# Optimization experiments

Hardware: AMD Instinct MI355X
Metric: run time of the kernel (lower is better)

The kernel has to match this reference:

```python
import jax, jax.numpy as jnp
import numpy as np

B, A, C, M, E = 8, 100000, 8, 128, 32
ALPHA, GAMMA = 0.25, 2.0


def setup_inputs() -> dict:
    key = jax.random.key(0)
    k1, k2, k3, k4, k5, k6, k7 = jax.random.split(key, 7)
    classifications = jax.random.uniform(k1, (B, A, C), dtype=jnp.float32)
    regressions = jax.random.normal(k2, (B, A, 8), dtype=jnp.float32)
    embeddings = jax.random.normal(k3, (B, A, E), dtype=jnp.float32)
    # anchors: random centers on a 1920x1080 image, reasonable w/h -> x1,y1,x2,y2
    cx = jax.random.uniform(k4, (A,), minval=0.0, maxval=1920.0)
    cy = jax.random.uniform(jax.random.fold_in(k4, 1), (A,), minval=0.0, maxval=1080.0)
    w = jax.random.uniform(jax.random.fold_in(k4, 2), (A,), minval=16.0, maxval=256.0)
    h = jax.random.uniform(jax.random.fold_in(k4, 3), (A,), minval=16.0, maxval=256.0)
    anchors = jnp.stack([cx - 0.5 * w, cy - 0.5 * h, cx + 0.5 * w, cy + 0.5 * h], axis=1)[None].astype(jnp.float32)
    # annotations: 16 coords = jittered 3D-box corner projections around a random box,
    # col 16 = object id, col 17 = class label in [0, C)
    bcx = jax.random.uniform(k5, (B, M, 1), minval=100.0, maxval=1820.0)
    bcy = jax.random.uniform(jax.random.fold_in(k5, 1), (B, M, 1), minval=100.0, maxval=980.0)
    bw = jax.random.uniform(jax.random.fold_in(k5, 2), (B, M, 1), minval=30.0, maxval=300.0)
    bh = jax.random.uniform(jax.random.fold_in(k5, 3), (B, M, 1), minval=30.0, maxval=300.0)
    jit = jax.random.uniform(k6, (B, M, 16), minval=-0.4, maxval=0.4)
    sx = jnp.array([-1, -1, 1, 1, -1, -1, 1, 1], jnp.float32)
    sy = jnp.array([-1, 1, -1, 1, -1, 1, -1, 1], jnp.float32)
    xs = bcx + 0.5 * bw * (sx + jit[..., 0:16:2])
    ys = bcy + 0.5 * bh * (sy + jit[..., 1:16:2])
    coords = jnp.stack([xs, ys], axis=-1).reshape(B, M, 16)
    ids = jax.random.randint(k7, (B, M, 1), 0, 1000).astype(jnp.float32)
    cls_lab = jax.random.randint(jax.random.fold_in(k7, 1), (B, M, 1), 0, C).astype(jnp.float32)
    annotations = jnp.concatenate([coords, ids, cls_lab], axis=-1)
    return {
        "classifications": classifications,
        "regressions": regressions,
        "anchors": anchors,
        "annotations": annotations,
        "embeddings": embeddings,
    }


def calc_iou(a, b):
    # a: [A,4], b: [M,4] in x1,y1,x2,y2 -> [A,M]
    area = (b[:, 2] - b[:, 0]) * (b[:, 3] - b[:, 1])
    iw = jnp.minimum(a[:, 2:3], b[None, :, 2]) - jnp.maximum(a[:, 0:1], b[None, :, 0])
    ih = jnp.minimum(a[:, 3:4], b[None, :, 3]) - jnp.maximum(a[:, 1:2], b[None, :, 1])
    iw = jnp.clip(iw, 0.0)
    ih = jnp.clip(ih, 0.0)
    ua = ((a[:, 2] - a[:, 0]) * (a[:, 3] - a[:, 1]))[:, None] + area[None, :] - iw * ih
    return iw * ih / jnp.clip(ua, 1e-8)


_S2 = jnp.array([-1, -1, 1, 1, -1, -1, 1, 1], jnp.float32)
_S4 = jnp.array([-1, 1, -1, 1, -1, 1, -1, 1], jnp.float32)
_S6 = jnp.array([1, 1, 1, 1, -1, -1, -1, -1], jnp.float32)


def _per_image(cls, reg, ann, anchor):
    # cls [A,C], reg [A,8], ann [M,18], anchor [A,4]
    aw = anchor[:, 2] - anchor[:, 0]
    ah = anchor[:, 3] - anchor[:, 1]
    acx = anchor[:, 0] + 0.5 * aw
    acy = anchor[:, 1] + 0.5 * ah
    cls = jnp.clip(cls, 1e-4, 1.0 - 1e-4)
    valid = ann[:, -1] >= 0.0  # [M]; annotations with class -1 are padding
    xs, ys = ann[:, 0:16:2], ann[:, 1:16:2]
    box2d = jnp.stack([xs.min(1), ys.min(1), xs.max(1), ys.max(1)], axis=1)  # [M,4]
    iou = jnp.where(valid[None, :], calc_iou(anchor, box2d), -1.0)  # [A,M]
    iou_max = iou.max(1)
    assigned = ann[iou.argmax(1)]  # [A,18]
    pos = iou_max >= 0.5
    neg = iou_max < 0.4
    num_pos = jnp.maximum(pos.sum().astype(cls.dtype), 1.0)

    onehot = jax.nn.one_hot(assigned[:, -1].astype(jnp.int32), cls.shape[1], dtype=cls.dtype)
    targets = jnp.where(pos[:, None], onehot, jnp.where(neg[:, None], 0.0, -1.0))
    alpha_f = jnp.where(targets == 1.0, ALPHA, 1.0 - ALPHA)
    focal_w = alpha_f * jnp.where(targets == 1.0, 1.0 - cls, cls) ** GAMMA
    bce = -(targets * jnp.log(cls) + (1.0 - targets) * jnp.log(1.0 - cls))
    cls_loss = jnp.where(targets != -1.0, focal_w * bce, 0.0).sum() / num_pos

    t = assigned[:, :16]

    def vp(rx, ry, tx, ty):
        denom = jnp.sqrt(rx * rx + ry * ry) * jnp.sqrt(tx * tx + ty * ty)
        return 1.0 - (rx * tx + ry * ty) / jnp.maximum(denom, 1e-8)

    vp1 = vp(reg[:, 2], reg[:, 3],
             (t[:, 4] + t[:, 6] + t[:, 12] + t[:, 14] - (t[:, 0] + t[:, 2] + t[:, 8] + t[:, 10])) / 4.0,
             (t[:, 5] + t[:, 7] + t[:, 13] + t[:, 15] - (t[:, 1] + t[:, 3] + t[:, 9] + t[:, 11])) / 4.0)
    vp2 = vp(reg[:, 4], reg[:, 5],
             (t[:, 2] + t[:, 6] + t[:, 10] + t[:, 14] - (t[:, 0] + t[:, 4] + t[:, 8] + t[:, 12])) / 4.0,
             (t[:, 3] + t[:, 7] + t[:, 11] + t[:, 15] - (t[:, 1] + t[:, 5] + t[:, 9] + t[:, 13])) / 4.0)
    vp3 = vp(reg[:, 6], reg[:, 7],
             (t[:, 0] + t[:, 2] + t[:, 4] + t[:, 6] - (t[:, 8] + t[:, 10] + t[:, 12] + t[:, 14])) / 4.0,
             (t[:, 1] + t[:, 3] + t[:, 5] + t[:, 7] - (t[:, 9] + t[:, 11] + t[:, 13] + t[:, 15])) / 4.0)
    vp_all = (vp1 + vp2 + vp3) / 3.0
    vp_loss = (vp_all * pos).sum() / num_pos

    # corner predictions from (ctr_x, ctr_y, v1, v2, v3) offsets: [A,8] x-coords, [A,8] y-coords
    px = reg[:, 0:1] + reg[:, 2:3] * _S2 + reg[:, 4:5] * _S4 + reg[:, 6:7] * _S6
    py = reg[:, 1:2] + reg[:, 3:4] * _S2 + reg[:, 5:6] * _S4 + reg[:, 7:8] * _S6
    tx = (t[:, 0:16:2] - acx[:, None]) / aw[:, None]
    ty = (t[:, 1:16:2] - acy[:, None]) / ah[:, None]
    diff = jnp.concatenate([jnp.abs(px - tx), jnp.abs(py - ty)], axis=1)  # [A,16]
    sl1 = jnp.where(diff <= 1.0 / 9.0, 0.5 * 9.0 * diff * diff, diff - 0.5 / 9.0)
    reg_loss = (sl1.mean(1) * pos).sum() / num_pos
    return cls_loss, reg_loss, vp_loss


def reference(classifications, regressions, anchors, annotations, embeddings):
    anchor = anchors[0]
    cls_l, reg_l, vp_l = jax.vmap(_per_image, in_axes=(0, 0, 0, None))(
        classifications, regressions, annotations, anchor)
    return jnp.stack([cls_l.mean(), reg_l.mean(), vp_l.mean()])


if __name__ == "__main__":
    print(reference(**setup_inputs()))
```

## Files before the change

kernel.cpp:

```cpp
#include <hip/hip_runtime.h>

namespace {

constexpr int B_N = 8;
constexpr int A_N = 100000;
constexpr int M_N = 128;
constexpr int BLOCK = 256;
constexpr int NBLK_S = (A_N + BLOCK - 1) / BLOCK;
constexpr int GX = 16, GY = 9, NC = GX * GY;
constexpr float CELL = 120.0f;
constexpr float MARGIN = 128.0f;
constexpr int CPC = 4;
constexpr int NCH = NC * CPC;

constexpr size_t OFF_BOX  = 0;
constexpr size_t OFF_MASK = OFF_BOX + (size_t)B_N * M_N * 8 * 4;
constexpr size_t OFF_HIST = OFF_MASK + (size_t)B_N * NC * 2 * 8;
constexpr size_t OFF_OFFS = OFF_HIST + (size_t)NBLK_S * NC * 4;
constexpr size_t OFF_CT   = OFF_OFFS + (size_t)NC * NBLK_S * 4;
constexpr size_t OFF_CB   = OFF_CT + NC * 4;
constexpr size_t OFF_SIDX = (OFF_CB + (NC + 1) * 4 + 15) & ~size_t(15);
constexpr size_t OFF_SANC = (OFF_SIDX + (size_t)A_N * 4 + 15) & ~size_t(15);
constexpr size_t OFF_PART = OFF_SANC + (size_t)A_N * 16;

__device__ __forceinline__ int cell_of(const float4& an) {
    const float acx = 0.5f * (an.x + an.z);
    const float acy = 0.5f * (an.y + an.w);
    const int cx = min(GX - 1, max(0, (int)(acx * (1.0f / CELL))));
    const int cy = min(GY - 1, max(0, (int)(acy * (1.0f / CELL))));
    return cy * GX + cx;
}

__global__ void k0_prep(const float* __restrict__ ann_, float* __restrict__ boxbuf)
{
    const int i = blockIdx.x * blockDim.x + threadIdx.x;
    if (i >= B_N * M_N) return;
    const float* t = ann_ + (size_t)i * 18;
    float minx = t[0], maxx = t[0], miny = t[1], maxy = t[1];
#pragma unroll
    for (int j = 1; j < 8; ++j) {
        const float xj = t[2 * j], yj = t[2 * j + 1];
        minx = fminf(minx, xj); maxx = fmaxf(maxx, xj);
        miny = fminf(miny, yj); maxy = fmaxf(maxy, yj);
    }
    float area = (maxx - minx) * (maxy - miny);
    if (t[17] < 0.0f) {
        minx = 1e30f; miny = 1e30f; maxx = -1e30f; maxy = -1e30f; area = 0.0f;
    }
    float* o = boxbuf + (size_t)i * 8;
    o[0] = minx; o[1] = miny; o[2] = maxx; o[3] = maxy;
    o[4] = area; o[5] = 0.f;  o[6] = 0.f;  o[7] = 0.f;
}

__global__ void kmask(const float* __restrict__ boxbuf,
                      unsigned long long* __restrict__ maskbuf)
{
    const int cell = blockIdx.x, b = blockIdx.y, m = threadIdx.x;
    const int cx = cell % GX, cy = cell / GX;
    const float lox = cx * CELL - MARGIN, hix = cx * CELL + CELL + MARGIN;
    const float loy = cy * CELL - MARGIN, hiy = cy * CELL + CELL + MARGIN;
    const float* r = boxbuf + ((size_t)b * M_N + m) * 8;
    const bool ok = (r[0] <= hix) && (r[2] >= lox) && (r[1] <= hiy) && (r[3] >= loy);
    const unsigned long long bal = __ballot(ok);
    if ((m & 63) == 0)
        maskbuf[((size_t)b * NC + cell) * 2 + (m >> 6)] = bal;
}

__global__ __launch_bounds__(BLOCK) void s1_hist(
    const float* __restrict__ anchors_, unsigned* __restrict__ hist)
{
    __shared__ unsigned h[NC];
    const int tid = threadIdx.x, blk = blockIdx.x;
    for (int i = tid; i < NC; i += BLOCK) h[i] = 0u;
    __syncthreads();
    const int a = blk * BLOCK + tid;
    if (a < A_N) {
        const float4 an = ((const float4*)anchors_)[a];
        atomicAdd(&h[cell_of(an)], 1u);
    }
    __syncthreads();
    for (int i = tid; i < NC; i += BLOCK) hist[(size_t)blk * NC + i] = h[i];
}

__global__ __launch_bounds__(BLOCK) void s2a_scan(
    const unsigned* __restrict__ hist,
    unsigned* __restrict__ offs,
    unsigned* __restrict__ cellTot)
{
    const int c = blockIdx.x, t = threadIdx.x;
    const int k0 = 2 * t, k1 = 2 * t + 1;
    const unsigned v0 = (k0 < NBLK_S) ? hist[(size_t)k0 * NC + c] : 0u;
    const unsigned v1 = (k1 < NBLK_S) ? hist[(size_t)k1 * NC + c] : 0u;
    const unsigned mysum = v0 + v1;
    __shared__ unsigned s[BLOCK];
    s[t] = mysum;
    __syncthreads();
    for (int off = 1; off < BLOCK; off <<= 1) {
        const unsigned x = (t >= off) ? s[t - off] : 0u;
        __syncthreads();
        s[t] += x;
        __syncthreads();
    }
    const unsigned excl = s[t] - mysum;
    if (k0 < NBLK_S) offs[(size_t)c * NBLK_S + k0] = excl;
    if (k1 < NBLK_S) offs[(size_t)c * NBLK_S + k1] = excl + v0;
    if (t == BLOCK - 1) cellTot[c] = s[BLOCK - 1];
}

__global__ __launch_bounds__(BLOCK) void s2b_base(
    const unsigned* __restrict__ cellTot, unsigned* __restrict__ cellBase)
{
    __shared__ unsigned s[BLOCK];
    const int t = threadIdx.x;
    const unsigned v = (t < NC) ? cellTot[t] : 0u;
    s[t] = v;
    __syncthreads();
    for (int off = 1; off < BLOCK; off <<= 1) {
        const unsigned x = (t >= off) ? s[t - off] : 0u;
        __syncthreads();
        s[t] += x;
        __syncthreads();
    }
    if (t < NC) cellBase[t] = s[t] - v;
    if (t == NC - 1) cellBase[NC] = s[t];
}

__global__ __launch_bounds__(BLOCK) void s3_scatter(
    const float* __restrict__ anchors_,
    const unsigned* __restrict__ offs, const unsigned* __restrict__ cellBase,
    unsigned* __restrict__ sidx, float4* __restrict__ sanc)
{
    __shared__ int cellArr[BLOCK];
    const int tid = threadIdx.x, blk = blockIdx.x;
    const int a = blk * BLOCK + tid;
    const bool v = (a < A_N);
    float4 an = make_float4(0.f, 0.f, 0.f, 0.f);
    int c = -1;
    if (v) { an = ((const float4*)anchors_)[a]; c = cell_of(an); }
    cellArr[tid] = c;
    __syncthreads();
    if (v) {
        int rank = 0;
        for (int j = 0; j < tid; ++j) rank += (cellArr[j] == c);
        const unsigned d = cellBase[c] + offs[(size_t)c * NBLK_S + blk] + (unsigned)rank;
        sidx[d] = (unsigned)a;
        sanc[d] = an;
    }
}

__global__ __launch_bounds__(BLOCK) void ka2(
    const float* __restrict__ cls_,
    const float* __restrict__ reg_,
    const float* __restrict__ ann_,
    const float* __restrict__ boxbuf,
    const unsigned* __restrict__ maskbuf,
    const unsigned* __restrict__ cellBase,
    const unsigned* __restrict__ sidx,
    const float4* __restrict__ sanc,
    float* __restrict__ partials)
{
    const int cc = blockIdx.x / CPC, chunk = blockIdx.x % CPC;
    const int b = blockIdx.y, tid = threadIdx.x;
    const int base = (int)cellBase[cc];
    const int n    = (int)cellBase[cc + 1] - base;

    if (chunk * BLOCK >= n) {
        if (tid == 0) {
            float* o = partials + ((size_t)b * NCH + blockIdx.x) * 4;
            o[0] = 0.f; o[1] = 0.f; o[2] = 0.f; o[3] = 0.f;
        }
        return;
    }

    __shared__ float s_x1[M_N], s_y1[M_N], s_x2[M_N], s_y2[M_N], s_nb[M_N];
    __shared__ int   s_id[M_N];
    __shared__ unsigned s_mask[4], s_pre[4];
    __shared__ int s_Kv;
    __shared__ float s_ann[M_N * 18];

    for (int i = tid; i < M_N * 18; i += BLOCK)
        s_ann[i] = ann_[(size_t)b * M_N * 18 + i];
    if (tid < 4) s_mask[tid] = maskbuf[((size_t)b * NC + cc) * 4 + tid];
    __syncthreads();
    if (tid == 0) {
        unsigned p = 0;
#pragma unroll
        for (int w = 0; w < 4; ++w) { s_pre[w] = p; p += __popc(s_mask[w]); }
        s_Kv = (int)p;
    }
    __syncthreads();
    if (tid < M_N) {
        const unsigned w = s_mask[tid >> 5];
        if ((w >> (tid & 31)) & 1u) {
            const int r = (int)(s_pre[tid >> 5] + __popc(w & ((1u << (tid & 31)) - 1u)));
            const float* rec = boxbuf + ((size_t)b * M_N + tid) * 8;
            s_x1[r] = rec[0]; s_y1[r] = rec[1];
            s_x2[r] = rec[2]; s_y2[r] = rec[3];
            s_nb[r] = -rec[4];
            s_id[r] = tid;
        }
    }
    __syncthreads();
    const int K = s_Kv;

    const int i0  = chunk * BLOCK + tid;
    const bool inb = (i0 < n);
    const int gi  = base + (inb ? i0 : 0);
    const float4 an = sanc[gi];
    const int a = (int)sidx[gi];

    const float* cp = cls_ + ((size_t)b * A_N + a) * 8;
    const float4 cA = ((const float4*)cp)[0];
    const float4 cB = ((const float4*)cp)[1];

    const float aarea = (an.z - an.x) * (an.w - an.y);
    float m1 = -3e38f, m2 = -3e38f;
    float bn = 0.f, bs = 1.f;
    int   kb = 0;

    for (int m = 0; m < K; ++m) {
        const float x1 = s_x1[m], y1 = s_y1[m];
        const float x2 = s_x2[m], y2 = s_y2[m];
        const float nb = s_nb[m];
        const float iw = fminf(an.z, x2) - fmaxf(an.x, x1);
        const float ih = fminf(an.w, y2) - fmaxf(an.y, y1);
        const float in_ = fmaxf(iw, 0.f) * fmaxf(ih, 0.f);
        m1 = fmaxf(m1, __builtin_fmaf(3.0f, in_, nb));
        m2 = fmaxf(m2, __builtin_fmaf(3.5f, in_, nb));
        const float s = aarea - nb;
        const bool  u = (in_ * bs > bn * s);
        bn = u ? in_ : bn;
        bs = u ? s   : bs;
        kb = u ? m   : kb;
    }

    const bool pos = inb && (m1 >= aarea);
    const bool nonign = pos || (m2 < aarea);

    float clsS = 0.f, regS = 0.f, vpS = 0.f, posC = 0.f;
    const float pv[8] = {cA.x, cA.y, cA.z, cA.w, cB.x, cB.y, cB.z, cB.w};
    {
        float s = 0.f;
#pragma unroll
        for (int c = 0; c < 8; ++c) {
            const float p = fminf(fmaxf(pv[c], 1e-4f), 1.0f - 1e-4f);
            s += 0.75f * p * p * (-__logf(1.0f - p));
        }
        clsS = (inb && nonign) ? s : 0.f;
    }

    if (pos) {
        posC = 1.0f;
        const float* t = s_ann + s_id[kb] * 18;
        float tt[16];
#pragma unroll
        for (int j = 0; j < 16; ++j) tt[j] = t[j];
        const int kc = (int)t[17];

        float pkc = 0.5f;
#pragma unroll
        for (int c = 0; c < 8; ++c)
            if (c == kc) pkc = fminf(fmaxf(pv[c], 1e-4f), 1.0f - 1e-4f);
        const float negkc   = 0.75f * pkc * pkc * (-__logf(1.0f - pkc));
        const float posterm = 0.25f * (1.0f - pkc) * (1.0f - pkc) * (-__logf(pkc));
        clsS += posterm - negkc;

        const float aw = an.z - an.x;
        const float ah = an.w - an.y;
        const float* rp = reg_ + ((size_t)b * A_N + a) * 8;
        const float4 r0 = ((const float4*)rp)[0];
        const float4 r1 = ((const float4*)rp)[1];

        auto vp = [](float rx, float ry, float tx, float ty) {
            const float denom = sqrtf(rx * rx + ry * ry) * sqrtf(tx * tx + ty * ty);
            return 1.0f - (rx * tx + ry * ty) / fmaxf(denom, 1e-8f);
        };
        const float vp1 = vp(r0.z, r0.w,
            (tt[4] + tt[6] + tt[12] + tt[14] - (tt[0] + tt[2] + tt[8] + tt[10])) * 0.25f,
            (tt[5] + tt[7] + tt[13] + tt[15] - (tt[1] + tt[3] + tt[9] + tt[11])) * 0.25f);
        const float vp2 = vp(r1.x, r1.y,
            (tt[2] + tt[6] + tt[10] + tt[14] - (tt[0] + tt[4] + tt[8] + tt[12])) * 0.25f,
            (tt[3] + tt[7] + tt[11] + tt[15] - (tt[1] + tt[5] + tt[9] + tt[13])) * 0.25f);
        const float vp3 = vp(r1.z, r1.w,
            (tt[0] + tt[2] + tt[4] + tt[6] - (tt[8] + tt[10] + tt[12] + tt[14])) * 0.25f,
            (tt[1] + tt[3] + tt[5] + tt[7] - (tt[9] + tt[11] + tt[13] + tt[15])) * 0.25f);
        vpS = (vp1 + vp2 + vp3) * (1.0f / 3.0f);

        const float s2v[8] = {-1, -1, 1, 1, -1, -1, 1, 1};
        const float s4v[8] = {-1, 1, -1, 1, -1, 1, -1, 1};
        const float s6v[8] = {1, 1, 1, 1, -1, -1, -1, -1};
        const float acx2 = an.x + 0.5f * aw;
        const float acy2 = an.y + 0.5f * ah;
        float ssum = 0.f;
#pragma unroll
        for (int j = 0; j < 8; ++j) {
            const float px = r0.x + r0.z * s2v[j] + r1.x * s4v[j] + r1.z * s6v[j];
            const float py = r0.y + r0.w * s2v[j] + r1.y * s4v[j] + r1.w * s6v[j];
            const float tx = (tt[2 * j]     - acx2) / aw;
            const float ty = (tt[2 * j + 1] - acy2) / ah;
            const float dx = fabsf(px - tx);
            const float dy = fabsf(py - ty);
            ssum += (dx <= (1.0f / 9.0f)) ? 4.5f * dx * dx : dx - (0.5f / 9.0f);
            ssum += (dy <= (1.0f / 9.0f)) ? 4.5f * dy * dy : dy - (0.5f / 9.0f);
        }
        regS = ssum * (1.0f / 16.0f);
    }

#pragma unroll
    for (int off = 32; off; off >>= 1) {
        clsS += __shfl_down(clsS, off);
        regS += __shfl_down(regS, off);
        vpS  += __shfl_down(vpS, off);
        posC += __shfl_down(posC, off);
    }
    __shared__ float s_red[4][4];
    const int wv = tid >> 6, ln = tid & 63;
    if (ln == 0) {
        s_red[wv][0] = clsS; s_red[wv][1] = regS;
        s_red[wv][2] = vpS;  s_red[wv][3] = posC;
    }
    __syncthreads();
    if (tid == 0) {
        float C = 0, R = 0, V = 0, P = 0;
        for (int w2 = 0; w2 < 4; ++w2) {
            C += s_red[w2][0]; R += s_red[w2][1];
            V += s_red[w2][2]; P += s_red[w2][3];
        }
        float* out = partials + ((size_t)b * NCH + blockIdx.x) * 4;
        out[0] = C; out[1] = R; out[2] = V; out[3] = P;
    }
}

__global__ __launch_bounds__(BLOCK) void kc_final(
    const float* __restrict__ partials,
    float* __restrict__ out)
{
    const int tid = threadIdx.x;
    __shared__ float s[4][4];
    __shared__ float accum[3];
    if (tid == 0) { accum[0] = 0.f; accum[1] = 0.f; accum[2] = 0.f; }

    for (int b = 0; b < B_N; ++b) {
        float c = 0.f, r = 0.f, v = 0.f, p = 0.f;
        for (int i = tid; i < NCH; i += BLOCK) {
            const float* q = partials + ((size_t)b * NCH + i) * 4;
            c += q[0]; r += q[1]; v += q[2]; p += q[3];
        }
#pragma unroll
        for (int off = 32; off; off >>= 1) {
            c += __shfl_down(c, off); r += __shfl_down(r, off);
            v += __shfl_down(v, off); p += __shfl_down(p, off);
        }
        const int wv = tid >> 6, ln = tid & 63;
        if (ln == 0) { s[wv][0] = c; s[wv][1] = r; s[wv][2] = v; s[wv][3] = p; }
        __syncthreads();
        if (tid == 0) {
            float C = 0, R = 0, V = 0, P = 0;
            for (int w = 0; w < 4; ++w) {
                C += s[w][0]; R += s[w][1]; V += s[w][2]; P += s[w][3];
            }
            const float np_ = fmaxf(P, 1.0f);
            accum[0] += C / np_; accum[1] += R / np_; accum[2] += V / np_;
        }
        __syncthreads();
    }
    if (tid == 0) {
        out[0] = accum[0] * 0.125f;
        out[1] = accum[1] * 0.125f;
        out[2] = accum[2] * 0.125f;
    }
}

}

extern "C" void kernel_launch(void* const* d_in, const int* in_sizes, int n_in,
                              void* d_out, int out_size, void* d_ws, size_t ws_size,
                              hipStream_t stream)
{
    const float* cls_    = (const float*)d_in[0];
    const float* reg_    = (const float*)d_in[1];
    const float* anchors = (const float*)d_in[2];
    const float* ann     = (const float*)d_in[3];

    char* ws = (char*)d_ws;
    float*              boxbuf  = (float*)(ws + OFF_BOX);
    unsigned long long* maskbuf = (unsigned long long*)(ws + OFF_MASK);
    unsigned*           hist    = (unsigned*)(ws + OFF_HIST);
    unsigned*           offs    = (unsigned*)(ws + OFF_OFFS);
    unsigned*           cellTot = (unsigned*)(ws + OFF_CT);
    unsigned*           cellBase= (unsigned*)(ws + OFF_CB);
    unsigned*           sidxp   = (unsigned*)(ws + OFF_SIDX);
    float4*             sancp   = (float4*)(ws + OFF_SANC);
    float*              partials= (float*)(ws + OFF_PART);

    k0_prep<<<dim3((B_N * M_N + BLOCK - 1) / BLOCK), dim3(BLOCK), 0, stream>>>(ann, boxbuf);
    kmask<<<dim3(NC, B_N), dim3(M_N), 0, stream>>>(boxbuf, maskbuf);
    s1_hist<<<dim3(NBLK_S), dim3(BLOCK), 0, stream>>>(anchors, hist);
    s2a_scan<<<dim3(NC), dim3(BLOCK), 0, stream>>>(hist, offs, cellTot);
    s2b_base<<<dim3(1), dim3(BLOCK), 0, stream>>>(cellTot, cellBase);
    s3_scatter<<<dim3(NBLK_S), dim3(BLOCK), 0, stream>>>(anchors, offs, cellBase,
                                                         sidxp, sancp);
    ka2<<<dim3(NCH, B_N), dim3(BLOCK), 0, stream>>>(
        cls_, reg_, ann, boxbuf, (const unsigned*)maskbuf, cellBase,
        sidxp, sancp, partials);
    kc_final<<<dim3(1), dim3(BLOCK), 0, stream>>>(partials, (float*)d_out);
}
```

Measured before the change: 71.78 us.

## Fuse prep/mask and base-scan kernels, use wave-shuffle ranking in scatter

Merges the annotation box prep into the mask kernel and folds the single-block cell base scan into every scatter block, which drops two kernel launches. Each scatter block now recomputes the scan redundantly, and block 0 writes cellBase for ka2. The O(tid) shared-memory rank loop is replaced by a 64-iteration wave shuffle plus per-wave counts. ka2 no longer stages all annotations into shared memory and instead reads the matched annotation row from global memory, which adds scattered global loads for positive anchors.

```diff
diff --git a/kernel.cpp b/kernel.cpp
--- a/kernel.cpp
+++ b/kernel.cpp
@@ -31,11 +31,12 @@
     return cy * GX + cx;
 }
 
-__global__ void k0_prep(const float* __restrict__ ann_, float* __restrict__ boxbuf)
-{
-    const int i = blockIdx.x * blockDim.x + threadIdx.x;
-    if (i >= B_N * M_N) return;
-    const float* t = ann_ + (size_t)i * 18;
+__global__ void f0_prep_mask(const float* __restrict__ ann_,
+                             float* __restrict__ boxbuf,
+                             unsigned long long* __restrict__ maskbuf)
+{
+    const int cell = blockIdx.x, b = blockIdx.y, m = threadIdx.x;
+    const float* t = ann_ + ((size_t)b * M_N + m) * 18;
     float minx = t[0], maxx = t[0], miny = t[1], maxy = t[1];
 #pragma unroll
     for (int j = 1; j < 8; ++j) {
@@ -47,20 +48,15 @@
     if (t[17] < 0.0f) {
         minx = 1e30f; miny = 1e30f; maxx = -1e30f; maxy = -1e30f; area = 0.0f;
     }
-    float* o = boxbuf + (size_t)i * 8;
-    o[0] = minx; o[1] = miny; o[2] = maxx; o[3] = maxy;
-    o[4] = area; o[5] = 0.f;  o[6] = 0.f;  o[7] = 0.f;
-}
-
-__global__ void kmask(const float* __restrict__ boxbuf,
-                      unsigned long long* __restrict__ maskbuf)
-{
-    const int cell = blockIdx.x, b = blockIdx.y, m = threadIdx.x;
+    if (cell == 0) {
+        float* o = boxbuf + ((size_t)b * M_N + m) * 8;
+        o[0] = minx; o[1] = miny; o[2] = maxx; o[3] = maxy;
+        o[4] = area; o[5] = 0.f;  o[6] = 0.f;  o[7] = 0.f;
+    }
     const int cx = cell % GX, cy = cell / GX;
     const float lox = cx * CELL - MARGIN, hix = cx * CELL + CELL + MARGIN;
     const float loy = cy * CELL - MARGIN, hiy = cy * CELL + CELL + MARGIN;
-    const float* r = boxbuf + ((size_t)b * M_N + m) * 8;
-    const bool ok = (r[0] <= hix) && (r[2] >= lox) && (r[1] <= hiy) && (r[3] >= loy);
+    const bool ok = (minx <= hix) && (maxx >= lox) && (miny <= hiy) && (maxy >= loy);
     const unsigned long long bal = __ballot(ok);
     if ((m & 63) == 0)
         maskbuf[((size_t)b * NC + cell) * 2 + (m >> 6)] = bal;
@@ -107,42 +103,54 @@
     if (t == BLOCK - 1) cellTot[c] = s[BLOCK - 1];
 }
 
-__global__ __launch_bounds__(BLOCK) void s2b_base(
-    const unsigned* __restrict__ cellTot, unsigned* __restrict__ cellBase)
-{
-    __shared__ unsigned s[BLOCK];
-    const int t = threadIdx.x;
-    const unsigned v = (t < NC) ? cellTot[t] : 0u;
-    s[t] = v;
-    __syncthreads();
-    for (int off = 1; off < BLOCK; off <<= 1) {
-        const unsigned x = (t >= off) ? s[t - off] : 0u;
-        __syncthreads();
-        s[t] += x;
-        __syncthreads();
-    }
-    if (t < NC) cellBase[t] = s[t] - v;
-    if (t == NC - 1) cellBase[NC] = s[t];
-}
-
 __global__ __launch_bounds__(BLOCK) void s3_scatter(
     const float* __restrict__ anchors_,
-    const unsigned* __restrict__ offs, const unsigned* __restrict__ cellBase,
+    const unsigned* __restrict__ offs,
+    const unsigned* __restrict__ cellTot,
+    unsigned* __restrict__ cellBase,
     unsigned* __restrict__ sidx, float4* __restrict__ sanc)
 {
-    __shared__ int cellArr[BLOCK];
+    __shared__ unsigned sscan[BLOCK];
+    __shared__ unsigned scb[NC];
+    __shared__ unsigned hw[4][NC];
     const int tid = threadIdx.x, blk = blockIdx.x;
+
+    const unsigned v = (tid < NC) ? cellTot[tid] : 0u;
+    sscan[tid] = v;
+    for (int i = tid; i < 4 * NC; i += BLOCK) (&hw[0][0])[i] = 0u;
+    __syncthreads();
+    for (int off = 1; off < BLOCK; off <<= 1) {
+        const unsigned x = (tid >= off) ? sscan[tid - off] : 0u;
+        __syncthreads();
+        sscan[tid] += x;
+        __syncthreads();
+    }
+    if (tid < NC) scb[tid] = sscan[tid] - v;
+    if (blk == 0) {
+        if (tid < NC) cellBase[tid] = sscan[tid] - v;
+        if (tid == NC - 1) cellBase[NC] = sscan[tid];
+    }
+
     const int a = blk * BLOCK + tid;
-    const bool v = (a < A_N);
+    const bool valid = (a < A_N);
     float4 an = make_float4(0.f, 0.f, 0.f, 0.f);
     int c = -1;
-    if (v) { an = ((const float4*)anchors_)[a]; c = cell_of(an); }
-    cellArr[tid] = c;
-    __syncthreads();
-    if (v) {
-        int rank = 0;
-        for (int j = 0; j < tid; ++j) rank += (cellArr[j] == c);
-        const unsigned d = cellBase[c] + offs[(size_t)c * NBLK_S + blk] + (unsigned)rank;
+    if (valid) { an = ((const float4*)anchors_)[a]; c = cell_of(an); }
+    const int ln = tid & 63, wv = tid >> 6;
+
+    int rank = 0, cnt = 0;
+    for (int j = 0; j < 64; ++j) {
+        const int cj = __shfl(c, j);
+        const bool same = (cj == c);
+        rank += (same && (j < ln));
+        cnt  += same;
+    }
+    if (valid && rank == 0) hw[wv][c] = (unsigned)cnt;
+    __syncthreads();
+    if (valid) {
+        unsigned r = (unsigned)rank;
+        for (int w = 0; w < wv; ++w) r += hw[w][c];
+        const unsigned d = scb[c] + offs[(size_t)c * NBLK_S + blk] + r;
         sidx[d] = (unsigned)a;
         sanc[d] = an;
     }
@@ -176,10 +184,7 @@
     __shared__ int   s_id[M_N];
     __shared__ unsigned s_mask[4], s_pre[4];
     __shared__ int s_Kv;
-    __shared__ float s_ann[M_N * 18];
-
-    for (int i = tid; i < M_N * 18; i += BLOCK)
-        s_ann[i] = ann_[(size_t)b * M_N * 18 + i];
+
     if (tid < 4) s_mask[tid] = maskbuf[((size_t)b * NC + cc) * 4 + tid];
     __syncthreads();
     if (tid == 0) {
@@ -251,7 +256,7 @@
 
     if (pos) {
         posC = 1.0f;
-        const float* t = s_ann + s_id[kb] * 18;
+        const float* t = ann_ + ((size_t)b * M_N + s_id[kb]) * 18;
         float tt[16];
 #pragma unroll
         for (int j = 0; j < 16; ++j) tt[j] = t[j];
@@ -393,13 +398,11 @@
     float4*             sancp   = (float4*)(ws + OFF_SANC);
     float*              partials= (float*)(ws + OFF_PART);
 
-    k0_prep<<<dim3((B_N * M_N + BLOCK - 1) / BLOCK), dim3(BLOCK), 0, stream>>>(ann, boxbuf);
-    kmask<<<dim3(NC, B_N), dim3(M_N), 0, stream>>>(boxbuf, maskbuf);
+    f0_prep_mask<<<dim3(NC, B_N), dim3(M_N), 0, stream>>>(ann, boxbuf, maskbuf);
     s1_hist<<<dim3(NBLK_S), dim3(BLOCK), 0, stream>>>(anchors, hist);
     s2a_scan<<<dim3(NC), dim3(BLOCK), 0, stream>>>(hist, offs, cellTot);
-    s2b_base<<<dim3(1), dim3(BLOCK), 0, stream>>>(cellTot, cellBase);
-    s3_scatter<<<dim3(NBLK_S), dim3(BLOCK), 0, stream>>>(anchors, offs, cellBase,
-                                                         sidxp, sancp);
+    s3_scatter<<<dim3(NBLK_S), dim3(BLOCK), 0, stream>>>(anchors, offs, cellTot,
+                                                         cellBase, sidxp, sancp);
     ka2<<<dim3(NCH, B_N), dim3(BLOCK), 0, stream>>>(
         cls_, reg_, ann, boxbuf, (const unsigned*)maskbuf, cellBase,
         sidxp, sancp, partials);
```

Measured after the change: 65.33 us. 9.0% less time.
